# Kernel optimization log

Measured on AMD Instinct MI355X. Metric: run time of the kernel, lower is better.

## Reference

```python
import jax, jax.numpy as jnp
import numpy as np

B, S, HID, NH, HD = 2, 2048, 1024, 16, 64
SCALE = 1.0 / np.sqrt(HD)
NEG = -1e9


def _rope_cache(seq_len, dim, base=10000.0):
    inv_freq = 1.0 / (base ** (np.arange(0, dim, 2, dtype=np.float32) / dim))
    t = np.arange(seq_len, dtype=np.float32)
    freqs = np.outer(t, inv_freq)                      # [S, dim/2]
    emb = np.concatenate([freqs, freqs], axis=-1)      # [S, dim]
    return jnp.asarray(np.cos(emb)), jnp.asarray(np.sin(emb))


def _rotate_half(x):
    x1, x2 = jnp.split(x, 2, axis=-1)
    return jnp.concatenate([-x2, x1], axis=-1)


def setup_inputs() -> dict:
    key = jax.random.key(0)
    k0, k1, k2, k3, k4 = jax.random.split(key, 5)
    hidden_states = jax.random.normal(k0, (B, S, HID), jnp.float32)
    Wq = jax.random.normal(k1, (HID, NH * HD), jnp.float32) * 0.02
    Wk = jax.random.normal(k2, (HID, NH * HD), jnp.float32) * 0.02
    Wv = jax.random.normal(k3, (HID, NH * HD), jnp.float32) * 0.02
    Wo = jax.random.normal(k4, (NH * HD, HID), jnp.float32) * 0.02
    causal = jnp.tril(jnp.ones((S, S), bool))
    attention_mask = jnp.broadcast_to(
        jnp.where(causal, 0.0, NEG).astype(jnp.float32)[None, None], (B, 1, S, S))
    position_ids = jnp.broadcast_to(jnp.arange(S, dtype=jnp.int32)[None], (B, S))
    cos, sin = _rope_cache(S, HD)
    return {"hidden_states": hidden_states, "attention_mask": attention_mask,
            "position_ids": position_ids, "cos": cos, "sin": sin,
            "Wq": Wq, "Wk": Wk, "Wv": Wv, "Wo": Wo}


def reference(hidden_states, attention_mask, position_ids, cos, sin, Wq, Wk, Wv, Wo):
    b, s, _ = hidden_states.shape
    def proj(W):  # [B,S,HID] @ [HID,NH*HD] -> [B,NH,S,HD]
        return jnp.einsum('bsh,hd->bsd', hidden_states, W).reshape(b, s, NH, HD).transpose(0, 2, 1, 3)
    q, k, v = proj(Wq), proj(Wk), proj(Wv)
    # RoPE: gather per-position cos/sin -> [B,1,S,HD]
    cos_g = cos[position_ids][:, None]
    sin_g = sin[position_ids][:, None]
    q = q * cos_g + _rotate_half(q) * sin_g
    k = k * cos_g + _rotate_half(k) * sin_g
    scores = jnp.einsum('bhqd,bhkd->bhqk', q, k) * SCALE + attention_mask
    attn = jax.nn.softmax(scores.astype(jnp.float32), axis=-1).astype(q.dtype)
    out = jnp.einsum('bhqk,bhkd->bhqd', attn, v)
    out = out.transpose(0, 2, 1, 3).reshape(b, s, NH * HD)
    return jnp.einsum('bsd,dh->bsh', out, Wo)
```

## Files before the change

### kernel.cpp

```cpp
#include <hip/hip_runtime.h>

typedef __bf16 bf16x8 __attribute__((ext_vector_type(8)));
typedef float  f32x4  __attribute__((ext_vector_type(4)));
typedef unsigned short ushortx8 __attribute__((ext_vector_type(8)));
typedef unsigned short ushortx4 __attribute__((ext_vector_type(4)));

static __device__ __forceinline__ unsigned short f2bf(float f) {
  unsigned int u = __builtin_bit_cast(unsigned int, f);
  u += 0x7FFFu + ((u >> 16) & 1u);
  return (unsigned short)(u >> 16);
}
static __device__ __forceinline__ unsigned short f2bf_fast(float f) {
  unsigned int u = __builtin_bit_cast(unsigned int, f);
  return (unsigned short)((u + 0x8000u) >> 16);
}

#define GLL16(gp, lp) __builtin_amdgcn_global_load_lds(                       \
    (const __attribute__((address_space(1))) void*)(gp),                      \
    (__attribute__((address_space(3))) void*)(lp), 16, 0, 0)

__global__ __launch_bounds__(256) void prep_kernel(const float* __restrict__ X,
                                                   const float* __restrict__ W0,
                                                   const float* __restrict__ W1,
                                                   const float* __restrict__ W2,
                                                   const float* __restrict__ W3,
                                                   unsigned short* __restrict__ Xbf,
                                                   unsigned short* __restrict__ D0,
                                                   unsigned short* __restrict__ D1,
                                                   unsigned short* __restrict__ D2,
                                                   unsigned short* __restrict__ D3) {
  int z = blockIdx.z;
  if (z >= 4) {
    long bid = (long)(z - 4) * 1024 + blockIdx.y * 32 + blockIdx.x;
    int tl = threadIdx.y * 32 + threadIdx.x;
    long i = bid * 2048 + (long)tl * 8;
    float4 f0 = *(const float4*)(X + i);
    float4 f1 = *(const float4*)(X + i + 4);
    ushortx8 u;
    u[0] = f2bf(f0.x); u[1] = f2bf(f0.y); u[2] = f2bf(f0.z); u[3] = f2bf(f0.w);
    u[4] = f2bf(f1.x); u[5] = f2bf(f1.y); u[6] = f2bf(f1.z); u[7] = f2bf(f1.w);
    *(ushortx8*)(Xbf + i) = u;
    return;
  }
  const float* src = (z == 0) ? W0 : (z == 1) ? W1 : (z == 2) ? W2 : W3;
  unsigned short* dst = (z == 0) ? D0 : (z == 1) ? D1 : (z == 2) ? D2 : D3;
  const int R = 1024, C = 1024;
  __shared__ unsigned short t[32][33];
  int c = blockIdx.x * 32 + threadIdx.x;
#pragma unroll
  for (int i = 0; i < 4; ++i) {
    int r = blockIdx.y * 32 + threadIdx.y + i * 8;
    t[threadIdx.y + i * 8][threadIdx.x] = f2bf(src[(size_t)r * C + c]);
  }
  __syncthreads();
  int rr = blockIdx.y * 32 + threadIdx.x;
#pragma unroll
  for (int i = 0; i < 4; ++i) {
    int cc = blockIdx.x * 32 + threadIdx.y + i * 8;
    dst[(size_t)cc * R + rr] = t[threadIdx.x][threadIdx.y + i * 8];
  }
}

__global__ __launch_bounds__(256, 3) void qkvr_kernel(
    const unsigned short* __restrict__ A,
    const unsigned short* __restrict__ BT0,
    const unsigned short* __restrict__ BT1,
    const unsigned short* __restrict__ BT2,
    unsigned short* __restrict__ outQ,
    unsigned short* __restrict__ outK,
    unsigned short* __restrict__ outVT,
    const int* __restrict__ pos_ids,
    const float* __restrict__ cosb,
    const float* __restrict__ sinb) {
  const int K = 1024;
  int id = blockIdx.x + 8 * (blockIdx.y + 32 * blockIdx.z);
  int m_idx = id & 31;
  int nzi = id >> 5;
  int n_idx = nzi & 7;
  int z = nzi >> 3;
  const unsigned short* BT = (z == 0) ? BT0 : (z == 1 ? BT1 : BT2);
  int n0 = n_idx * 128, m0 = m_idx * 128;
  int t = threadIdx.x, lane = t & 63, w = t >> 6;
  int wy = w >> 1, wx = w & 1;
  int n16 = lane & 15, quad = lane >> 4;

  __shared__ __align__(16) unsigned short sA[3][128][32];
  __shared__ __align__(16) unsigned short sB[3][128][32];
  __shared__ __align__(16) unsigned short sDummy[512];
  const int BUFE = 128 * 32;

  int r4 = lane >> 2, c4 = lane & 3;
  const char* gA = (const char*)(A + (size_t)(m0 + w * 32 + r4) * K) + ((c4 ^ (r4 & 3)) * 16);
  const char* gB = (const char*)(BT + (size_t)(n0 + w * 32 + r4) * K) + ((c4 ^ (r4 & 3)) * 16);
  const size_t row16 = (size_t)16 * K * 2;
  unsigned short* stA = &sA[0][w * 32][0];
  unsigned short* stB = &sB[0][w * 32][0];

  int cs = (quad ^ (n16 & 3)) * 8;
  const unsigned short* rdA = &sA[0][wy * 64 + n16][0] + cs;
  const unsigned short* rdB = &sB[0][wx * 64 + n16][0] + cs;

  f32x4 acc[4][4];
#pragma unroll
  for (int i = 0; i < 4; ++i)
#pragma unroll
    for (int j = 0; j < 4; ++j) acc[i][j] = f32x4{0.f, 0.f, 0.f, 0.f};

  bf16x8 a[4], b[4];

#define QSTG(tt, dA, dB)                                                        \
  do {                                                                          \
    GLL16(gA + (size_t)(tt) * 64, (dA));                                        \
    GLL16(gA + (size_t)(tt) * 64 + row16, (dA) + 16 * 32);                      \
    GLL16(gB + (size_t)(tt) * 64, (dB));                                        \
    GLL16(gB + (size_t)(tt) * 64 + row16, (dB) + 16 * 32);                      \
  } while (0)

#define QRD(bufi)                                                               \
  do {                                                                          \
    _Pragma("unroll") for (int i = 0; i < 4; ++i) {                             \
      a[i] = *(const bf16x8*)(rdA + (bufi) * BUFE + (i * 16) * 32);             \
      b[i] = *(const bf16x8*)(rdB + (bufi) * BUFE + (i * 16) * 32);             \
    }                                                                           \
  } while (0)

#define QMM                                                                     \
  do {                                                                          \
    _Pragma("unroll") for (int mt = 0; mt < 4; ++mt)                            \
      _Pragma("unroll") for (int nt = 0; nt < 4; ++nt)                          \
        acc[mt][nt] = __builtin_amdgcn_mfma_f32_16x16x32_bf16(                  \
            a[mt], b[nt], acc[mt][nt], 0, 0, 0);                                \
  } while (0)

  QSTG(0, stA, stB);
  QSTG(1, stA + BUFE, stB + BUFE);
  asm volatile("s_waitcnt vmcnt(4)" ::: "memory");
  __builtin_amdgcn_s_barrier();

#pragma unroll 3
  for (int kt = 0; kt < 30; ++kt) {
    int buf = kt % 3;
    int pfb = (kt + 2) % 3;
    QRD(buf);
    QSTG(kt + 2, stA + pfb * BUFE, stB + pfb * BUFE);
    QMM;
    asm volatile("s_waitcnt vmcnt(4)" ::: "memory");
    __builtin_amdgcn_s_barrier();
  }
  {
    QRD(0);
    QSTG(31, sDummy, sDummy);
    QMM;
    asm volatile("s_waitcnt vmcnt(4)" ::: "memory");
    __builtin_amdgcn_s_barrier();
  }
  {
    QRD(1);
    QSTG(31, sDummy, sDummy);
    QMM;
    asm volatile("s_waitcnt vmcnt(0)" ::: "memory");
  }
#undef QSTG
#undef QRD
#undef QMM

  if (z < 2) {
    const float qs = (z == 0) ? (0.125f * 1.44269504088896340736f) : 1.0f;
#pragma unroll
    for (int mt = 0; mt < 4; ++mt)
#pragma unroll
      for (int r = 0; r < 4; ++r) {
        int row = m0 + wy * 64 + mt * 16 + quad * 4 + r;
        int b_ = row >> 11, s_ = row & 2047;
        int pos = pos_ids[b_ * 2048 + s_];
        const float* cb = cosb + (size_t)pos * 64;
        const float* sb = sinb + (size_t)pos * 64;
#pragma unroll
        for (int nt = 0; nt < 2; ++nt) {
          int d0 = nt * 16 + n16;
          float c0 = cb[d0] * qs, s0 = sb[d0] * qs;
          float c1 = cb[d0 + 32] * qs, s1 = sb[d0 + 32] * qs;
          float x0 = acc[mt][nt][r], x1 = acc[mt][nt + 2][r];
          acc[mt][nt][r]     = x0 * c0 - x1 * s0;
          acc[mt][nt + 2][r] = x1 * c1 + x0 * s1;
        }
      }
    unsigned short* dst = (z == 0) ? outQ : outK;
#pragma unroll
    for (int mt = 0; mt < 4; ++mt)
#pragma unroll
      for (int nt = 0; nt < 4; ++nt)
#pragma unroll
        for (int r = 0; r < 4; ++r) {
          int row = m0 + wy * 64 + mt * 16 + quad * 4 + r;
          int col = n0 + wx * 64 + nt * 16 + n16;
          int b_ = row >> 11, s_ = row & 2047, h_ = col >> 6, d_ = col & 63;
          dst[(((size_t)b_ * 16 + h_) * 2048 + s_) * 64 + d_] = f2bf(acc[mt][nt][r]);
        }
    return;
  }

#pragma unroll
  for (int mt = 0; mt < 4; ++mt)
#pragma unroll
    for (int nt = 0; nt < 4; ++nt) {
      int row = m0 + wy * 64 + mt * 16 + quad * 4;
      int b_ = row >> 11, s_ = row & 2047;
      int col = n0 + wx * 64 + nt * 16 + n16;
      int h_ = col >> 6, d_ = col & 63;
      ushortx4 u;
#pragma unroll
      for (int r = 0; r < 4; ++r) u[r] = f2bf(acc[mt][nt][r]);
      *(ushortx4*)(&outVT[(((size_t)b_ * 16 + h_) * 64 + d_) * 2048 + s_]) = u;
    }
}

__global__ __launch_bounds__(256) void wor_kernel(const unsigned short* __restrict__ A,
                                                  const unsigned short* __restrict__ BT,
                                                  float* __restrict__ outF) {
  const int K = 1024, N = 1024;
  int id = blockIdx.x + 8 * blockIdx.y;
  int m_idx = id & 31, n_idx = id >> 5;
  int m0 = m_idx * 128, n0 = n_idx * 64;
  int t = threadIdx.x, lane = t & 63, w = t >> 6;
  int wy = w >> 1, wx = w & 1;
  int n16 = lane & 15, quad = lane >> 4;

  __shared__ __align__(16) unsigned short sA[3][128][32];
  __shared__ __align__(16) unsigned short sB[3][64][32];
  __shared__ __align__(16) unsigned short sDummy[512];
  const int BUFA = 128 * 32, BUFB = 64 * 32;

  int r4 = lane >> 2, c4 = lane & 3;
  const char* gA = (const char*)(A + (size_t)(m0 + w * 32 + r4) * K) + ((c4 ^ (r4 & 3)) * 16);
  const char* gB = (const char*)(BT + (size_t)(n0 + w * 16 + r4) * K) + ((c4 ^ (r4 & 3)) * 16);
  const size_t row16 = (size_t)16 * K * 2;
  unsigned short* stA = &sA[0][w * 32][0];
  unsigned short* stB = &sB[0][w * 16][0];

  int cs = (quad ^ (n16 & 3)) * 8;
  const unsigned short* rdA = &sA[0][wy * 64 + n16][0] + cs;
  const unsigned short* rdB = &sB[0][wx * 32 + n16][0] + cs;

  f32x4 acc[4][2];
#pragma unroll
  for (int i = 0; i < 4; ++i)
#pragma unroll
    for (int j = 0; j < 2; ++j) acc[i][j] = f32x4{0.f, 0.f, 0.f, 0.f};

  bf16x8 a[4], b[2];

#define WSTG(tt, dA, dB)                                                        \
  do {                                                                          \
    GLL16(gA + (size_t)(tt) * 64, (dA));                                        \
    GLL16(gA + (size_t)(tt) * 64 + row16, (dA) + 16 * 32);                      \
    GLL16(gB + (size_t)(tt) * 64, (dB));                                        \
  } while (0)

#define WRD(bufi)                                                               \
  do {                                                                          \
    _Pragma("unroll") for (int i = 0; i < 4; ++i)                               \
      a[i] = *(const bf16x8*)(rdA + (bufi) * BUFA + (i * 16) * 32);             \
    _Pragma("unroll") for (int j = 0; j < 2; ++j)                               \
      b[j] = *(const bf16x8*)(rdB + (bufi) * BUFB + (j * 16) * 32);             \
  } while (0)

#define WMM                                                                     \
  do {                                                                          \
    _Pragma("unroll") for (int mt = 0; mt < 4; ++mt)                            \
      _Pragma("unroll") for (int nt = 0; nt < 2; ++nt)                          \
        acc[mt][nt] = __builtin_amdgcn_mfma_f32_16x16x32_bf16(                  \
            a[mt], b[nt], acc[mt][nt], 0, 0, 0);                                \
  } while (0)

  WSTG(0, stA, stB);
  WSTG(1, stA + BUFA, stB + BUFB);
  asm volatile("s_waitcnt vmcnt(3)" ::: "memory");
  __builtin_amdgcn_s_barrier();

#pragma unroll 3
  for (int kt = 0; kt < 30; ++kt) {
    int buf = kt % 3;
    int pfb = (kt + 2) % 3;
    WRD(buf);
    WSTG(kt + 2, stA + pfb * BUFA, stB + pfb * BUFB);
    WMM;
    asm volatile("s_waitcnt vmcnt(3)" ::: "memory");
    __builtin_amdgcn_s_barrier();
  }
  {
    WRD(0);
    WSTG(31, sDummy, sDummy);
    WMM;
    asm volatile("s_waitcnt vmcnt(3)" ::: "memory");
    __builtin_amdgcn_s_barrier();
  }
  {
    WRD(1);
    WSTG(31, sDummy, sDummy);
    WMM;
    asm volatile("s_waitcnt vmcnt(0)" ::: "memory");
  }
#undef WSTG
#undef WRD
#undef WMM

#pragma unroll
  for (int mt = 0; mt < 4; ++mt)
#pragma unroll
    for (int nt = 0; nt < 2; ++nt)
#pragma unroll
      for (int r = 0; r < 4; ++r) {
        int row = m0 + wy * 64 + mt * 16 + quad * 4 + r;
        int col = n0 + wx * 32 + nt * 16 + n16;
        outF[(size_t)row * N + col] = acc[mt][nt][r];
      }
}

__global__ __launch_bounds__(256) void attn_kernel(const unsigned short* __restrict__ Q,
                                                   const unsigned short* __restrict__ Kk,
                                                   const unsigned short* __restrict__ VT,
                                                   unsigned short* __restrict__ O) {
  int bh = blockIdx.x;
  int qt = (int)(gridDim.y - 1 - blockIdx.y);
  int t = threadIdx.x;
  int lane = t & 63;
  int w = t >> 6;
  int n16 = lane & 15, quad = lane >> 4;
  int r8 = lane >> 3, c8 = lane & 7;
  const unsigned short* Qb = Q + (size_t)bh * 2048 * 64;
  const unsigned short* Kb = Kk + (size_t)bh * 2048 * 64;
  const unsigned short* Vb = VT + (size_t)bh * 64 * 2048;

  __shared__ __align__(16) unsigned short sKV[2 * 8192];
  __shared__ __align__(16) unsigned short sP[4][16 * 64];
  unsigned short* spW = sP[w];

  int b_ = bh >> 4, h_ = bh & 15;
  int nk = qt + 1;
  int qg = qt * 64 + w * 16 + n16;

  bf16x8 aQ[2];
#pragma unroll
  for (int kb = 0; kb < 2; ++kb)
    aQ[kb] = *(const bf16x8*)(Qb + (size_t)qg * 64 + kb * 32 + quad * 8);

  f32x4 o[4];
  float mst = -3e38f, lst = 0.f;
#pragma unroll
  for (int ct = 0; ct < 4; ++ct) o[ct] = f32x4{0.f, 0.f, 0.f, 0.f};

#define ASTAGE(kt_, BUF)                                                                  \
  do {                                                                                    \
    const unsigned short* kg_ = Kb + (size_t)((kt_) * 64 + w * 16) * 64;                  \
    const unsigned short* vg_ = Vb + (size_t)(w * 16) * 2048 + (kt_) * 64;                \
    unsigned short* dK = sKV + (BUF) * 8192 + (w * 16) * 64;                              \
    unsigned short* dV = dK + 4096;                                                       \
    GLL16(kg_ + (size_t)r8 * 64 + (c8 ^ r8) * 8, dK);                                     \
    GLL16(kg_ + (size_t)(8 + r8) * 64 + (c8 ^ r8) * 8, dK + 8 * 64);                      \
    GLL16(vg_ + (size_t)r8 * 2048 + (c8 ^ r8) * 8, dV);                                   \
    GLL16(vg_ + (size_t)(8 + r8) * 2048 + (c8 ^ r8) * 8, dV + 8 * 64);                    \
  } while (0)

#define ACOMPUTE(kt_, BUF)                                                                \
  do {                                                                                    \
    const unsigned short* kT_ = sKV + (BUF) * 8192;                                       \
    const unsigned short* vT_ = kT_ + 4096;                                               \
    f32x4 sc[4];                                \
    _Pragma("unroll") for (int mt = 0; mt < 4; ++mt) {                                    \
      const unsigned short* kr = &kT_[(mt * 16 + n16) * 64];                              \
      bf16x8 ka0 = *(const bf16x8*)(kr + ((quad ^ (n16 & 7)) * 8));                       \
      bf16x8 ka1 = *(const bf16x8*)(kr + (((4 + quad) ^ (n16 & 7)) * 8));                 \
      f32x4 zv = f32x4{0.f, 0.f, 0.f, 0.f};                                               \
      zv = __builtin_amdgcn_mfma_f32_16x16x32_bf16(ka0, aQ[0], zv, 0, 0, 0);              \
      sc[mt] = __builtin_amdgcn_mfma_f32_16x16x32_bf16(ka1, aQ[1], zv, 0, 0, 0);          \
    }                                                                                     \
    float p[4][4];                                                                        \
    _Pragma("unroll") for (int mt = 0; mt < 4; ++mt)                                      \
      _Pragma("unroll") for (int r = 0; r < 4; ++r) p[mt][r] = sc[mt][r];                 \
    if ((kt_) == nk - 1) {                                 \
      int kb0 = (kt_) * 64 + quad * 4;                                                    \
      _Pragma("unroll") for (int mt = 0; mt < 4; ++mt)                                    \
        _Pragma("unroll") for (int r = 0; r < 4; ++r)                                     \
          if (kb0 + mt * 16 + r > qg) p[mt][r] = -3e38f;                                  \
    }                                                                                     \
    float rm = p[0][0];                                                                   \
    _Pragma("unroll") for (int mt = 0; mt < 4; ++mt)                                      \
      _Pragma("unroll") for (int r = 0; r < 4; ++r) rm = fmaxf(rm, p[mt][r]);             \
    rm = fmaxf(rm, __shfl_xor(rm, 16));                                                   \
    rm = fmaxf(rm, __shfl_xor(rm, 32));                                                   \
    if (!__all(rm <= mst + 8.f)) {        \
      float mn = fmaxf(mst, rm);                                                          \
      float al = exp2f(mst - mn);                                                         \
      mst = mn;                                                                           \
      lst *= al;                                                                          \
      _Pragma("unroll") for (int ct = 0; ct < 4; ++ct)                                    \
        _Pragma("unroll") for (int r = 0; r < 4; ++r) o[ct][r] *= al;                     \
    }                                                                                     \
    float rs = 0.f;                                                                       \
    _Pragma("unroll") for (int mt = 0; mt < 4; ++mt)                                      \
      _Pragma("unroll") for (int r = 0; r < 4; ++r) {                                     \
        p[mt][r] = exp2f(p[mt][r] - mst);                                                 \
        rs += p[mt][r];                                                                   \
      }                                                                                   \
    lst += rs;                                                                            \
    _Pragma("unroll") for (int mt = 0; mt < 4; ++mt) {                                    \
      ushortx4 uu;                                                                        \
      _Pragma("unroll") for (int r = 0; r < 4; ++r) uu[r] = f2bf_fast(p[mt][r]);          \
      int ch = (mt * 2 + (quad >> 1)) ^ (n16 & 7);                                        \
      *(ushortx4*)(&spW[n16 * 64 + ch * 8 + (quad & 1) * 4]) = uu;                        \
    }                                                                                     \
    __builtin_amdgcn_s_waitcnt(0xC07F);     \
    bf16x8 aP0 = *(const bf16x8*)(&spW[n16 * 64 + ((quad ^ (n16 & 7)) * 8)]);             \
    bf16x8 aP1 = *(const bf16x8*)(&spW[n16 * 64 + (((4 + quad) ^ (n16 & 7)) * 8)]);       \
    _Pragma("unroll") for (int ct = 0; ct < 4; ++ct) {                                    \
      const unsigned short* vr = &vT_[(ct * 16 + n16) * 64];                              \
      bf16x8 va0 = *(const bf16x8*)(vr + ((quad ^ (n16 & 7)) * 8));                       \
      bf16x8 va1 = *(const bf16x8*)(vr + (((4 + quad) ^ (n16 & 7)) * 8));                 \
      o[ct] = __builtin_amdgcn_mfma_f32_16x16x32_bf16(va0, aP0, o[ct], 0, 0, 0);          \
      o[ct] = __builtin_amdgcn_mfma_f32_16x16x32_bf16(va1, aP1, o[ct], 0, 0, 0);          \
    }                                                                                     \
  } while (0)

  ASTAGE(0, 0);
  int it = 0;
  while (it < nk) {
    __syncthreads();
    {
      int kt = it;
      if (kt + 1 < nk) ASTAGE(kt + 1, 1);
      ACOMPUTE(kt, 0);
    }
    if (++it >= nk) break;
    __syncthreads();
    {
      int kt = it;
      if (kt + 1 < nk) ASTAGE(kt + 1, 0);
      ACOMPUTE(kt, 1);
    }
    ++it;
  }
#undef ASTAGE
#undef ACOMPUTE

  lst += __shfl_xor(lst, 16);
  lst += __shfl_xor(lst, 32);
  float inv = 1.0f / lst;
#pragma unroll
  for (int ct = 0; ct < 4; ++ct) {
    ushortx4 uo;
#pragma unroll
    for (int r = 0; r < 4; ++r) uo[r] = f2bf(o[ct][r] * inv);
    size_t addr = ((size_t)b_ * 2048 + qg) * 1024 + h_ * 64 + ct * 16 + quad * 4;
    *(ushortx4*)(&O[addr]) = uo;
  }
}

extern "C" void kernel_launch(void* const* d_in, const int* in_sizes, int n_in,
                              void* d_out, int out_size, void* d_ws, size_t ws_size,
                              hipStream_t stream) {
  const float* X    = (const float*)d_in[0];
  const int*   pos  = (const int*)d_in[2];
  const float* cosb = (const float*)d_in[3];
  const float* sinb = (const float*)d_in[4];
  const float* Wq   = (const float*)d_in[5];
  const float* Wk   = (const float*)d_in[6];
  const float* Wv   = (const float*)d_in[7];
  const float* Wo   = (const float*)d_in[8];
  float* out = (float*)d_out;

  char* ws = (char*)d_ws;
  const size_t SZ_X = 4096UL * 1024 * 2;
  const size_t SZ_W = 1024UL * 1024 * 2;
  unsigned short* Xbf = (unsigned short*)(ws);
  unsigned short* WTq = (unsigned short*)(ws + SZ_X);
  unsigned short* WTk = (unsigned short*)(ws + SZ_X + SZ_W);
  unsigned short* WTv = (unsigned short*)(ws + SZ_X + 2 * SZ_W);
  unsigned short* WTo = (unsigned short*)(ws + SZ_X + 3 * SZ_W);
  unsigned short* Qbf = (unsigned short*)(ws + SZ_X + 4 * SZ_W);
  unsigned short* Kbf = (unsigned short*)(ws + 2 * SZ_X + 4 * SZ_W);
  unsigned short* VTr = (unsigned short*)(ws + 3 * SZ_X + 4 * SZ_W);
  unsigned short* Obf = (unsigned short*)(ws + 4 * SZ_X + 4 * SZ_W);

  prep_kernel<<<dim3(32, 32, 6), dim3(32, 8), 0, stream>>>(
      X, Wq, Wk, Wv, Wo, Xbf, WTq, WTk, WTv, WTo);

  qkvr_kernel<<<dim3(8, 32, 3), 256, 0, stream>>>(Xbf, WTq, WTk, WTv,
                                                  Qbf, Kbf, VTr,
                                                  pos, cosb, sinb);

  attn_kernel<<<dim3(32, 32), 256, 0, stream>>>(Qbf, Kbf, VTr, Obf);

  wor_kernel<<<dim3(8, 64), 256, 0, stream>>>(Obf, WTo, out);
}
```

Baseline: 201.6 us.

## Process two 64-row query tiles per attention block to reuse K/V tiles

Each attention block now covers 128 query rows by giving every warp two 16-row query slices that share each staged K/V tile from LDS. Online-softmax state, P buffers and output accumulators are duplicated per slice, and the grid's query dimension is halved. The aim is to halve K/V global-to-LDS traffic per query and add MFMA work that can overlap within a warp. The cost is higher register and LDS pressure, fewer blocks for the causal load balance, and the first slice computing one fully masked key tile per block.

```diff
diff --git a/kernel.cpp b/kernel.cpp
--- a/kernel.cpp
+++ b/kernel.cpp
@@ -322,7 +322,7 @@
                                                    const unsigned short* __restrict__ VT,
                                                    unsigned short* __restrict__ O) {
   int bh = blockIdx.x;
-  int qt = (int)(gridDim.y - 1 - blockIdx.y);
+  int qt = 15 - (int)blockIdx.y;
   int t = threadIdx.x;
   int lane = t & 63;
   int w = t >> 6;
@@ -333,22 +333,29 @@
   const unsigned short* Vb = VT + (size_t)bh * 64 * 2048;
 
   __shared__ __align__(16) unsigned short sKV[2 * 8192];
-  __shared__ __align__(16) unsigned short sP[4][16 * 64];
-  unsigned short* spW = sP[w];
+  __shared__ __align__(16) unsigned short sP[4][2][16 * 64];
+  unsigned short* spW0 = sP[w][0];
+  unsigned short* spW1 = sP[w][1];
 
   int b_ = bh >> 4, h_ = bh & 15;
-  int nk = qt + 1;
-  int qg = qt * 64 + w * 16 + n16;
-
-  bf16x8 aQ[2];
-#pragma unroll
-  for (int kb = 0; kb < 2; ++kb)
-    aQ[kb] = *(const bf16x8*)(Qb + (size_t)qg * 64 + kb * 32 + quad * 8);
-
-  f32x4 o[4];
-  float mst = -3e38f, lst = 0.f;
-#pragma unroll
-  for (int ct = 0; ct < 4; ++ct) o[ct] = f32x4{0.f, 0.f, 0.f, 0.f};
+  int nk = 2 * qt + 2;
+  int qg0 = qt * 128 + w * 16 + n16;
+  int qg1 = qg0 + 64;
+
+  bf16x8 aQ0[2], aQ1[2];
+#pragma unroll
+  for (int kb = 0; kb < 2; ++kb) {
+    aQ0[kb] = *(const bf16x8*)(Qb + (size_t)qg0 * 64 + kb * 32 + quad * 8);
+    aQ1[kb] = *(const bf16x8*)(Qb + (size_t)qg1 * 64 + kb * 32 + quad * 8);
+  }
+
+  f32x4 o0[4], o1[4];
+  float mst0 = -3e38f, lst0 = 0.f, mst1 = -3e38f, lst1 = 0.f;
+#pragma unroll
+  for (int ct = 0; ct < 4; ++ct) {
+    o0[ct] = f32x4{0.f, 0.f, 0.f, 0.f};
+    o1[ct] = f32x4{0.f, 0.f, 0.f, 0.f};
+  }
 
 #define ASTAGE(kt_, BUF)                                                                  \
   do {                                                                                    \
@@ -362,63 +369,76 @@
     GLL16(vg_ + (size_t)(8 + r8) * 2048 + (c8 ^ r8) * 8, dV + 8 * 64);                    \
   } while (0)
 
-#define ACOMPUTE(kt_, BUF)                                                                \
+#define SOFTMAX_SUB(SC, QG, MASKC, MST, LST, OO, SPW)                                     \
   do {                                                                                    \
-    const unsigned short* kT_ = sKV + (BUF) * 8192;                                       \
-    const unsigned short* vT_ = kT_ + 4096;                                               \
-    f32x4 sc[4];                                \
-    _Pragma("unroll") for (int mt = 0; mt < 4; ++mt) {                                    \
-      const unsigned short* kr = &kT_[(mt * 16 + n16) * 64];                              \
-      bf16x8 ka0 = *(const bf16x8*)(kr + ((quad ^ (n16 & 7)) * 8));                       \
-      bf16x8 ka1 = *(const bf16x8*)(kr + (((4 + quad) ^ (n16 & 7)) * 8));                 \
-      f32x4 zv = f32x4{0.f, 0.f, 0.f, 0.f};                                               \
-      zv = __builtin_amdgcn_mfma_f32_16x16x32_bf16(ka0, aQ[0], zv, 0, 0, 0);              \
-      sc[mt] = __builtin_amdgcn_mfma_f32_16x16x32_bf16(ka1, aQ[1], zv, 0, 0, 0);          \
-    }                                                                                     \
     float p[4][4];                                                                        \
     _Pragma("unroll") for (int mt = 0; mt < 4; ++mt)                                      \
-      _Pragma("unroll") for (int r = 0; r < 4; ++r) p[mt][r] = sc[mt][r];                 \
-    if ((kt_) == nk - 1) {                                 \
+      _Pragma("unroll") for (int r = 0; r < 4; ++r) p[mt][r] = SC[mt][r];                 \
+    if (MASKC) {                                                                          \
       int kb0 = (kt_) * 64 + quad * 4;                                                    \
       _Pragma("unroll") for (int mt = 0; mt < 4; ++mt)                                    \
         _Pragma("unroll") for (int r = 0; r < 4; ++r)                                     \
-          if (kb0 + mt * 16 + r > qg) p[mt][r] = -3e38f;                                  \
+          if (kb0 + mt * 16 + r > (QG)) p[mt][r] = -3e38f;                                \
     }                                                                                     \
     float rm = p[0][0];                                                                   \
     _Pragma("unroll") for (int mt = 0; mt < 4; ++mt)                                      \
       _Pragma("unroll") for (int r = 0; r < 4; ++r) rm = fmaxf(rm, p[mt][r]);             \
     rm = fmaxf(rm, __shfl_xor(rm, 16));                                                   \
     rm = fmaxf(rm, __shfl_xor(rm, 32));                                                   \
-    if (!__all(rm <= mst + 8.f)) {        \
-      float mn = fmaxf(mst, rm);                                                          \
-      float al = exp2f(mst - mn);                                                         \
-      mst = mn;                                                                           \
-      lst *= al;                                                                          \
+    if (!__all(rm <= MST + 8.f)) {                                     \
+      float mn = fmaxf(MST, rm);                                                          \
+      float al = exp2f(MST - mn);                                                         \
+      MST = mn;                                                                           \
+      LST *= al;                                                                          \
       _Pragma("unroll") for (int ct = 0; ct < 4; ++ct)                                    \
-        _Pragma("unroll") for (int r = 0; r < 4; ++r) o[ct][r] *= al;                     \
+        _Pragma("unroll") for (int r = 0; r < 4; ++r) OO[ct][r] *= al;                    \
     }                                                                                     \
     float rs = 0.f;                                                                       \
     _Pragma("unroll") for (int mt = 0; mt < 4; ++mt)                                      \
       _Pragma("unroll") for (int r = 0; r < 4; ++r) {                                     \
-        p[mt][r] = exp2f(p[mt][r] - mst);                                                 \
+        p[mt][r] = exp2f(p[mt][r] - MST);                                                 \
         rs += p[mt][r];                                                                   \
       }                                                                                   \
-    lst += rs;                                                                            \
+    LST += rs;                                                                            \
     _Pragma("unroll") for (int mt = 0; mt < 4; ++mt) {                                    \
       ushortx4 uu;                                                                        \
       _Pragma("unroll") for (int r = 0; r < 4; ++r) uu[r] = f2bf_fast(p[mt][r]);          \
       int ch = (mt * 2 + (quad >> 1)) ^ (n16 & 7);                                        \
-      *(ushortx4*)(&spW[n16 * 64 + ch * 8 + (quad & 1) * 4]) = uu;                        \
+      *(ushortx4*)(&(SPW)[n16 * 64 + ch * 8 + (quad & 1) * 4]) = uu;                      \
     }                                                                                     \
+  } while (0)
+
+#define ACOMPUTE2(kt_, BUF)                                                               \
+  do {                                                                                    \
+    const unsigned short* kT_ = sKV + (BUF) * 8192;                                       \
+    const unsigned short* vT_ = kT_ + 4096;                                               \
+    f32x4 sc0[4], sc1[4];                                                                 \
+    _Pragma("unroll") for (int mt = 0; mt < 4; ++mt) {                                    \
+      const unsigned short* kr = &kT_[(mt * 16 + n16) * 64];                              \
+      bf16x8 ka0 = *(const bf16x8*)(kr + ((quad ^ (n16 & 7)) * 8));                       \
+      bf16x8 ka1 = *(const bf16x8*)(kr + (((4 + quad) ^ (n16 & 7)) * 8));                 \
+      f32x4 z0 = f32x4{0.f, 0.f, 0.f, 0.f};                                               \
+      z0 = __builtin_amdgcn_mfma_f32_16x16x32_bf16(ka0, aQ0[0], z0, 0, 0, 0);             \
+      sc0[mt] = __builtin_amdgcn_mfma_f32_16x16x32_bf16(ka1, aQ0[1], z0, 0, 0, 0);        \
+      f32x4 z1 = f32x4{0.f, 0.f, 0.f, 0.f};                                               \
+      z1 = __builtin_amdgcn_mfma_f32_16x16x32_bf16(ka0, aQ1[0], z1, 0, 0, 0);             \
+      sc1[mt] = __builtin_amdgcn_mfma_f32_16x16x32_bf16(ka1, aQ1[1], z1, 0, 0, 0);        \
+    }                                                                                     \
+    SOFTMAX_SUB(sc0, qg0, (kt_) >= nk - 2, mst0, lst0, o0, spW0);                         \
+    SOFTMAX_SUB(sc1, qg1, (kt_) == nk - 1, mst1, lst1, o1, spW1);                         \
     __builtin_amdgcn_s_waitcnt(0xC07F);     \
-    bf16x8 aP0 = *(const bf16x8*)(&spW[n16 * 64 + ((quad ^ (n16 & 7)) * 8)]);             \
-    bf16x8 aP1 = *(const bf16x8*)(&spW[n16 * 64 + (((4 + quad) ^ (n16 & 7)) * 8)]);       \
+    bf16x8 aP00 = *(const bf16x8*)(&spW0[n16 * 64 + ((quad ^ (n16 & 7)) * 8)]);           \
+    bf16x8 aP01 = *(const bf16x8*)(&spW0[n16 * 64 + (((4 + quad) ^ (n16 & 7)) * 8)]);     \
+    bf16x8 aP10 = *(const bf16x8*)(&spW1[n16 * 64 + ((quad ^ (n16 & 7)) * 8)]);           \
+    bf16x8 aP11 = *(const bf16x8*)(&spW1[n16 * 64 + (((4 + quad) ^ (n16 & 7)) * 8)]);     \
     _Pragma("unroll") for (int ct = 0; ct < 4; ++ct) {                                    \
       const unsigned short* vr = &vT_[(ct * 16 + n16) * 64];                              \
       bf16x8 va0 = *(const bf16x8*)(vr + ((quad ^ (n16 & 7)) * 8));                       \
       bf16x8 va1 = *(const bf16x8*)(vr + (((4 + quad) ^ (n16 & 7)) * 8));                 \
-      o[ct] = __builtin_amdgcn_mfma_f32_16x16x32_bf16(va0, aP0, o[ct], 0, 0, 0);          \
-      o[ct] = __builtin_amdgcn_mfma_f32_16x16x32_bf16(va1, aP1, o[ct], 0, 0, 0);          \
+      o0[ct] = __builtin_amdgcn_mfma_f32_16x16x32_bf16(va0, aP00, o0[ct], 0, 0, 0);       \
+      o0[ct] = __builtin_amdgcn_mfma_f32_16x16x32_bf16(va1, aP01, o0[ct], 0, 0, 0);       \
+      o1[ct] = __builtin_amdgcn_mfma_f32_16x16x32_bf16(va0, aP10, o1[ct], 0, 0, 0);       \
+      o1[ct] = __builtin_amdgcn_mfma_f32_16x16x32_bf16(va1, aP11, o1[ct], 0, 0, 0);       \
     }                                                                                     \
   } while (0)
 
@@ -427,32 +447,40 @@
   while (it < nk) {
     __syncthreads();
     {
-      int kt = it;
-      if (kt + 1 < nk) ASTAGE(kt + 1, 1);
-      ACOMPUTE(kt, 0);
+      int kt_ = it;
+      if (kt_ + 1 < nk) ASTAGE(kt_ + 1, 1);
+      ACOMPUTE2(kt_, 0);
     }
     if (++it >= nk) break;
     __syncthreads();
     {
-      int kt = it;
-      if (kt + 1 < nk) ASTAGE(kt + 1, 0);
-      ACOMPUTE(kt, 1);
+      int kt_ = it;
+      if (kt_ + 1 < nk) ASTAGE(kt_ + 1, 0);
+      ACOMPUTE2(kt_, 1);
     }
     ++it;
   }
 #undef ASTAGE
-#undef ACOMPUTE
-
-  lst += __shfl_xor(lst, 16);
-  lst += __shfl_xor(lst, 32);
-  float inv = 1.0f / lst;
+#undef SOFTMAX_SUB
+#undef ACOMPUTE2
+
+  lst0 += __shfl_xor(lst0, 16);
+  lst0 += __shfl_xor(lst0, 32);
+  lst1 += __shfl_xor(lst1, 16);
+  lst1 += __shfl_xor(lst1, 32);
+  float inv0 = 1.0f / lst0, inv1 = 1.0f / lst1;
 #pragma unroll
   for (int ct = 0; ct < 4; ++ct) {
-    ushortx4 uo;
-#pragma unroll
-    for (int r = 0; r < 4; ++r) uo[r] = f2bf(o[ct][r] * inv);
-    size_t addr = ((size_t)b_ * 2048 + qg) * 1024 + h_ * 64 + ct * 16 + quad * 4;
-    *(ushortx4*)(&O[addr]) = uo;
+    ushortx4 u0, u1;
+#pragma unroll
+    for (int r = 0; r < 4; ++r) {
+      u0[r] = f2bf(o0[ct][r] * inv0);
+      u1[r] = f2bf(o1[ct][r] * inv1);
+    }
+    size_t a0 = ((size_t)b_ * 2048 + qg0) * 1024 + h_ * 64 + ct * 16 + quad * 4;
+    size_t a1 = ((size_t)b_ * 2048 + qg1) * 1024 + h_ * 64 + ct * 16 + quad * 4;
+    *(ushortx4*)(&O[a0]) = u0;
+    *(ushortx4*)(&O[a1]) = u1;
   }
 }
 
@@ -489,7 +517,7 @@
                                                   Qbf, Kbf, VTr,
                                                   pos, cosb, sinb);
 
-  attn_kernel<<<dim3(32, 32), 256, 0, stream>>>(Qbf, Kbf, VTr, Obf);
+  attn_kernel<<<dim3(32, 16), 256, 0, stream>>>(Qbf, Kbf, VTr, Obf);
 
   wor_kernel<<<dim3(8, 64), 256, 0, stream>>>(Obf, WTo, out);
 }
```

Measured after the change: 215.8 us. 1.07x slower.
